# Kernel tuning notes

Hardware: AMD Instinct MI355X
Metric: run time of the kernel (lower is better)

## Reference

```python
import jax, jax.numpy as jnp
import numpy as np
import math

D_MODEL = 256
NUM_HEADS = 8
D_HEAD = 32
K_EIG = 32
NUM_BANDS = 3


def setup_inputs() -> dict:
    key = jax.random.key(0)
    ks = jax.random.split(key, 12)
    B, N = 2, 50000
    x = jax.random.normal(ks[0], (B, N, D_MODEL), dtype=jnp.float32)
    eigenvectors = jax.random.normal(ks[1], (N, K_EIG), dtype=jnp.float32) / np.sqrt(N)
    eigenvalues = jnp.sort(jax.random.uniform(ks[2], (K_EIG,), dtype=jnp.float32))
    s = 1.0 / np.sqrt(D_MODEL)
    Wq = jax.random.normal(ks[3], (NUM_HEADS * D_HEAD, D_MODEL), dtype=jnp.float32) * s
    bq = jnp.zeros((NUM_HEADS * D_HEAD,), dtype=jnp.float32)
    Wk = jax.random.normal(ks[4], (NUM_HEADS * D_HEAD, D_MODEL), dtype=jnp.float32) * s
    bk = jnp.zeros((NUM_HEADS * D_HEAD,), dtype=jnp.float32)
    Wv = jax.random.normal(ks[5], (NUM_HEADS * D_HEAD, D_MODEL), dtype=jnp.float32) * s
    bv = jnp.zeros((NUM_HEADS * D_HEAD,), dtype=jnp.float32)
    # per-head SpectralFilter params
    band_boundaries = jnp.tile(jnp.linspace(0.0, 1.0, NUM_BANDS + 1, dtype=jnp.float32)[None, :], (NUM_HEADS, 1))
    filter_weights = jnp.ones((NUM_HEADS, NUM_BANDS, K_EIG), dtype=jnp.float32) + 0.1 * jax.random.normal(ks[6], (NUM_HEADS, NUM_BANDS, K_EIG), dtype=jnp.float32)
    return {"x": x, "eigenvectors": eigenvectors, "eigenvalues": eigenvalues,
            "Wq": Wq, "bq": bq, "Wk": Wk, "bk": bk, "Wv": Wv, "bv": bv,
            "band_boundaries": band_boundaries, "filter_weights": filter_weights}


def _filter_responses(eigenvalues, band_boundaries, filter_weights):
    # eigenvalues [K]; band_boundaries [H, NB+1]; filter_weights [H, NB, K] -> [H, K]
    lam = (eigenvalues - eigenvalues.min()) / (eigenvalues.max() - eigenvalues.min() + 1e-8)  # [K]
    resp = jnp.zeros(filter_weights.shape[::2], dtype=eigenvalues.dtype)  # [H, K]
    for i in range(NUM_BANDS):  # small fixed loop; later bands overwrite (faithful to torch)
        lo = band_boundaries[:, i:i + 1]   # [H,1]
        hi = band_boundaries[:, i + 1:i + 2]
        mask = (lam[None, :] >= lo) & (lam[None, :] < hi)  # [H,K]
        resp = jnp.where(mask, filter_weights[:, i, :], resp)
    return resp


def reference(x, eigenvectors, eigenvalues, Wq, bq, Wk, bk, Wv, bv, band_boundaries, filter_weights):
    B, N, D = x.shape
    H, Dh = NUM_HEADS, D_HEAD
    Q = (x @ Wq.T + bq).reshape(B, N, H, Dh)
    K = (x @ Wk.T + bk).reshape(B, N, H, Dh)
    V = (x @ Wv.T + bv).reshape(B, N, H, Dh)
    # project to spectral domain: [B,K,H,Dh]
    Qf = jnp.einsum('nk,bnhd->bkhd', eigenvectors, Q)
    Kf = jnp.einsum('nk,bnhd->bkhd', eigenvectors, K)
    Vf = jnp.einsum('nk,bnhd->bkhd', eigenvectors, V)
    resp = _filter_responses(eigenvalues, band_boundaries, filter_weights)  # [H,K]
    g = resp.T[None, :, :, None]  # [1,K,H,1]
    Qf, Kf, Vf = Qf * g, Kf * g, Vf * g
    scores = jnp.einsum('bkhd,blhd->bkhl', Qf, Kf) / math.sqrt(Dh)  # [B,K,H,K]
    attn = jax.nn.softmax(scores, axis=-1)
    out_freq = jnp.einsum('bkhl,blhd->bkhd', attn, Vf)
    out = jnp.einsum('nk,bkhd->bnhd', eigenvectors, out_freq)
    return out.reshape(B, N, H * Dh)
```

## Files before the change

### kernel.cpp

```cpp
#include <hip/hip_runtime.h>
#include <hip/hip_bf16.h>


constexpr int D = 256;

__global__ __launch_bounds__(256) void k_colsum(const float* __restrict__ E,
                                                float* __restrict__ pS, int N) {
  int k = threadIdx.x & 31;
  int rg = threadIdx.x >> 5;
  int rs = (N + 255) >> 8;
  int n0 = blockIdx.x * rs;
  int n1 = n0 + rs; if (n1 > N) n1 = N;
  float acc = 0.f;
  for (int n = n0 + rg; n < n1; n += 8) acc += E[(size_t)n * 32 + k];
  __shared__ float red[256];
  red[threadIdx.x] = acc;
  __syncthreads();
  if (threadIdx.x < 32) {
    float t = red[threadIdx.x];
#pragma unroll
    for (int i = 1; i < 8; ++i) t += red[i * 32 + threadIdx.x];
    pS[blockIdx.x * 32 + threadIdx.x] = t;
  }
}

__global__ __launch_bounds__(256) void k_partial(const float* __restrict__ x,
                                                 const float* __restrict__ E,
                                                 float* __restrict__ pU,
                                                 int N, int nchunk, int rpc) {
  int blk = blockIdx.x;
  int dh = blk & 1;
  int bc = blk >> 1;
  int c = bc % nchunk;
  int b = bc / nchunk;
  int t = threadIdx.x;
  int ro = t >> 6;
  int lane = t & 63;
  int n0 = c * rpc;
  int n1 = n0 + rpc; if (n1 > N) n1 = N;
  int nrows = n1 - n0; if (nrows < 0) nrows = 0;

  __shared__ __align__(16) float smem[4096];

  if (nrows > 0) {
    const float4* Esrc = reinterpret_cast<const float4*>(E + (size_t)n0 * 32);
    float4* Edst = reinterpret_cast<float4*>(smem);
    int nf4 = nrows * 8;
    for (int i = t; i < nf4; i += 256) Edst[i] = Esrc[i];
  }
  __syncthreads();

  float2 a0={0,0},a1={0,0},a2={0,0},a3={0,0},a4={0,0},a5={0,0},a6={0,0},a7={0,0};
  float2 a8={0,0},a9={0,0},a10={0,0},a11={0,0},a12={0,0},a13={0,0},a14={0,0},a15={0,0};
  float2 a16={0,0},a17={0,0},a18={0,0},a19={0,0},a20={0,0},a21={0,0},a22={0,0},a23={0,0};
  float2 a24={0,0},a25={0,0},a26={0,0},a27={0,0},a28={0,0},a29={0,0},a30={0,0},a31={0,0};

  int mrows = (nrows > ro) ? ((nrows - ro + 3) >> 2) : 0;

  if (mrows > 0) {
    const float* xb = x + (size_t)b * N * D + dh * 128 + 2 * lane;
#define XLD(j) (*reinterpret_cast<const float2*>( \
    xb + (size_t)(n0 + ro + 4 * ((j) < mrows ? (j) : mrows - 1)) * D))

    float2 p0 = XLD(0), p1 = XLD(1), p2 = XLD(2), p3 = XLD(3);
    float2 p4 = XLD(4), p5 = XLD(5), p6 = XLD(6), p7 = XLD(7);

#define FMAK(e, aA, aB, aC, aD)                                   \
  aA.x = fmaf(e.x, xq.x, aA.x); aA.y = fmaf(e.x, xq.y, aA.y);     \
  aB.x = fmaf(e.y, xq.x, aB.x); aB.y = fmaf(e.y, xq.y, aB.y);     \
  aC.x = fmaf(e.z, xq.x, aC.x); aC.y = fmaf(e.z, xq.y, aC.y);     \
  aD.x = fmaf(e.w, xq.x, aD.x); aD.y = fmaf(e.w, xq.y, aD.y);

#define ROW1(j, q) {                                              \
    const float4* eb = reinterpret_cast<const float4*>(           \
        smem + (ro + 4 * (j)) * 32);                              \
    float4 e0 = eb[0], e1 = eb[1], e2 = eb[2], e3 = eb[3];        \
    float4 e4 = eb[4], e5 = eb[5], e6 = eb[6], e7 = eb[7];        \
    float2 xq = q;                                                \
    FMAK(e0, a0,  a1,  a2,  a3)  FMAK(e1, a4,  a5,  a6,  a7)      \
    FMAK(e2, a8,  a9,  a10, a11) FMAK(e3, a12, a13, a14, a15)     \
    FMAK(e4, a16, a17, a18, a19) FMAK(e5, a20, a21, a22, a23)     \
    FMAK(e6, a24, a25, a26, a27) FMAK(e7, a28, a29, a30, a31) }

    int j = 0;
#pragma unroll 1
    for (; j + 8 <= mrows; j += 8) {
      ROW1(j + 0, p0) ROW1(j + 1, p1) ROW1(j + 2, p2) ROW1(j + 3, p3)
      p0 = XLD(j + 8);  p1 = XLD(j + 9);  p2 = XLD(j + 10); p3 = XLD(j + 11);
      ROW1(j + 4, p4) ROW1(j + 5, p5) ROW1(j + 6, p6) ROW1(j + 7, p7)
      p4 = XLD(j + 12); p5 = XLD(j + 13); p6 = XLD(j + 14); p7 = XLD(j + 15);
    }
    int rem = mrows - j;
    if (rem > 0) ROW1(j + 0, p0)
    if (rem > 1) ROW1(j + 1, p1)
    if (rem > 2) ROW1(j + 2, p2)
    if (rem > 3) ROW1(j + 3, p3)
    if (rem > 4) ROW1(j + 4, p4)
    if (rem > 5) ROW1(j + 5, p5)
    if (rem > 6) ROW1(j + 6, p6)
#undef ROW1
#undef FMAK
#undef XLD
  }

  float2* rb = reinterpret_cast<float2*>(smem);
  float* o = pU + ((size_t)bc * 2 + dh) * 4096;

#define OCT(g, cA, cB, cC, cD, cE, cF, cG, cH)                    \
  __syncthreads();                                                \
  rb[(ro * 8 + 0) * 64 + lane] = cA; rb[(ro * 8 + 1) * 64 + lane] = cB; \
  rb[(ro * 8 + 2) * 64 + lane] = cC; rb[(ro * 8 + 3) * 64 + lane] = cD; \
  rb[(ro * 8 + 4) * 64 + lane] = cE; rb[(ro * 8 + 5) * 64 + lane] = cF; \
  rb[(ro * 8 + 6) * 64 + lane] = cG; rb[(ro * 8 + 7) * 64 + lane] = cH; \
  __syncthreads();                                                \
  _Pragma("unroll")                                               \
  for (int i = 0; i < 2; ++i) {                                   \
    int idx = i * 256 + t;                                        \
    int kk = idx >> 6, ll = idx & 63;                             \
    float2 s0 = rb[(0 * 8 + kk) * 64 + ll], s1 = rb[(1 * 8 + kk) * 64 + ll]; \
    float2 s2 = rb[(2 * 8 + kk) * 64 + ll], s3 = rb[(3 * 8 + kk) * 64 + ll]; \
    float2 sv;                                                    \
    sv.x = (s0.x + s1.x) + (s2.x + s3.x);                         \
    sv.y = (s0.y + s1.y) + (s2.y + s3.y);                         \
    *reinterpret_cast<float2*>(o + ((g) * 8 + kk) * 128 + 2 * ll) = sv; \
  }

  OCT(0, a0,  a1,  a2,  a3,  a4,  a5,  a6,  a7)
  OCT(1, a8,  a9,  a10, a11, a12, a13, a14, a15)
  OCT(2, a16, a17, a18, a19, a20, a21, a22, a23)
  OCT(3, a24, a25, a26, a27, a28, a29, a30, a31)
#undef OCT
}

__global__ __launch_bounds__(256) void k_reduce(const float* __restrict__ pU,
                                                float* __restrict__ U, int nchunk) {
  int e = blockIdx.x * 32 + (threadIdx.x & 31);
  int sub = threadIdx.x >> 5;
  int b = e >> 13;
  int kd = e & 8191;
  int k = kd >> 8;
  int d = kd & 255;
  int dh = d >> 7, dl = d & 127;
  const float* p = pU + (size_t)b * nchunk * 8192 + (size_t)dh * 4096 + k * 128 + dl;
  float a0 = 0.f, a1 = 0.f, a2 = 0.f, a3 = 0.f;
  float a4 = 0.f, a5 = 0.f, a6 = 0.f, a7 = 0.f;
  int c = sub;
#pragma unroll 1
  for (; c + 56 < nchunk; c += 64) {
    a0 += p[(size_t)c * 8192];
    a1 += p[(size_t)(c + 8) * 8192];
    a2 += p[(size_t)(c + 16) * 8192];
    a3 += p[(size_t)(c + 24) * 8192];
    a4 += p[(size_t)(c + 32) * 8192];
    a5 += p[(size_t)(c + 40) * 8192];
    a6 += p[(size_t)(c + 48) * 8192];
    a7 += p[(size_t)(c + 56) * 8192];
  }
  for (; c < nchunk; c += 8) a0 += p[(size_t)c * 8192];
  __shared__ float red[256];
  red[threadIdx.x] = ((a0 + a1) + (a2 + a3)) + ((a4 + a5) + (a6 + a7));
  __syncthreads();
  if (threadIdx.x < 32) {
    float s = red[threadIdx.x];
#pragma unroll
    for (int i = 1; i < 8; ++i) s += red[i * 32 + threadIdx.x];
    U[e] = s;
  }
}

__global__ __launch_bounds__(256) void k_project(
    const float* __restrict__ U, const float* __restrict__ pS,
    const float* __restrict__ Wq, const float* __restrict__ bq,
    const float* __restrict__ Wk, const float* __restrict__ bk,
    const float* __restrict__ Wv, const float* __restrict__ bv,
    const float* __restrict__ ev, const float* __restrict__ bb,
    const float* __restrict__ fw,
    float* __restrict__ Qfg, float* __restrict__ Kfg, float* __restrict__ Vfg) {
  int blk = blockIdx.x;
  int k = blk & 31;
  int t = threadIdx.x;
  __shared__ __align__(16) float u[256];
  __shared__ float red[256];
  u[t] = U[(size_t)blk * 256 + t];
  red[t] = pS[t * 32 + k];
  __syncthreads();
#pragma unroll
  for (int off = 128; off > 0; off >>= 1) {
    if (t < off) red[t] += red[t + off];
    __syncthreads();
  }
  float sk = red[0];

  float mnf = ev[0], mxf = ev[0];
#pragma unroll
  for (int i = 1; i < 32; ++i) { float v = ev[i]; mnf = fminf(mnf, v); mxf = fmaxf(mxf, v); }
  double mn = (double)mnf, mx = (double)mxf;
  double lam = ((double)ev[k] - mn) / (mx - mn + 1e-8);
  int h = t >> 5;
  float g = 0.f;
#pragma unroll
  for (int i = 0; i < 3; ++i) {
    double lo = (double)bb[h * 4 + i], hi = (double)bb[h * 4 + i + 1];
    if (lam >= lo && lam < hi) g = fw[(h * 3 + i) * 32 + k];
  }

  const float4* u4 = reinterpret_cast<const float4*>(u);
  const float4* wq4 = reinterpret_cast<const float4*>(Wq) + (size_t)t * 64;
  const float4* wk4 = reinterpret_cast<const float4*>(Wk) + (size_t)t * 64;
  const float4* wv4 = reinterpret_cast<const float4*>(Wv) + (size_t)t * 64;
  float aq = 0.f, ak = 0.f, av = 0.f;
#pragma unroll 4
  for (int j = 0; j < 64; ++j) {
    float4 uv = u4[j];
    float4 q = wq4[j], kk = wk4[j], vv = wv4[j];
    aq = fmaf(uv.x, q.x, aq);  aq = fmaf(uv.y, q.y, aq);
    aq = fmaf(uv.z, q.z, aq);  aq = fmaf(uv.w, q.w, aq);
    ak = fmaf(uv.x, kk.x, ak); ak = fmaf(uv.y, kk.y, ak);
    ak = fmaf(uv.z, kk.z, ak); ak = fmaf(uv.w, kk.w, ak);
    av = fmaf(uv.x, vv.x, av); av = fmaf(uv.y, vv.y, av);
    av = fmaf(uv.z, vv.z, av); av = fmaf(uv.w, vv.w, av);
  }
  Qfg[(size_t)blk * 256 + t] = (aq + bq[t] * sk) * g;
  Kfg[(size_t)blk * 256 + t] = (ak + bk[t] * sk) * g;
  Vfg[(size_t)blk * 256 + t] = (av + bv[t] * sk) * g;
}

__global__ __launch_bounds__(1024) void k_attn(const float* __restrict__ Qfg,
                                               const float* __restrict__ Kfg,
                                               const float* __restrict__ Vfg,
                                               float* __restrict__ of) {
  int blk = blockIdx.x;
  int b = blk >> 3, h = blk & 7;
  int tid = threadIdx.x;
  int row = tid >> 5, col = tid & 31;
  __shared__ float Q[32][33], Kt[32][33], V[32][33], A[32][33];
  size_t base = (size_t)b * 32 * 256 + h * 32;
  Q[row][col]  = Qfg[base + row * 256 + col];
  Kt[row][col] = Kfg[base + row * 256 + col];
  V[row][col]  = Vfg[base + row * 256 + col];
  __syncthreads();
  float sc = 0.f;
#pragma unroll
  for (int d0 = 0; d0 < 32; ++d0) sc = fmaf(Q[row][d0], Kt[col][d0], sc);
  sc *= 0.17677669529663687f;
  float m = sc;
#pragma unroll
  for (int o = 16; o > 0; o >>= 1) m = fmaxf(m, __shfl_xor(m, o, 32));
  float p = expf(sc - m);
  float su = p;
#pragma unroll
  for (int o = 16; o > 0; o >>= 1) su += __shfl_xor(su, o, 32);
  A[row][col] = p / su;
  __syncthreads();
  float o_ = 0.f;
#pragma unroll
  for (int l = 0; l < 32; ++l) o_ = fmaf(A[row][l], V[l][col], o_);
  of[base + row * 256 + col] = o_;
}

__global__ __launch_bounds__(256) void k_expand(const float* __restrict__ E,
                                                const float* __restrict__ of,
                                                float* __restrict__ out,
                                                int N, int rows) {
  int n0 = blockIdx.x * rows;
  int n1 = n0 + rows; if (n1 > N) n1 = N;
  int nrows = n1 - n0;
  if (nrows <= 0) return;
  int t = threadIdx.x;

  const float* ofb = of + t;
#define LDF(i) float2 f##i = make_float2(ofb[(i) * 256], ofb[8192 + (i) * 256]);
  LDF(0)  LDF(1)  LDF(2)  LDF(3)  LDF(4)  LDF(5)  LDF(6)  LDF(7)
  LDF(8)  LDF(9)  LDF(10) LDF(11) LDF(12) LDF(13) LDF(14) LDF(15)
  LDF(16) LDF(17) LDF(18) LDF(19) LDF(20) LDF(21) LDF(22) LDF(23)
  LDF(24) LDF(25) LDF(26) LDF(27) LDF(28) LDF(29) LDF(30) LDF(31)
#undef LDF

  __shared__ __align__(16) float Elds[50 * 32];
  {
    const float4* Esrc = reinterpret_cast<const float4*>(E + (size_t)n0 * 32);
    float4* Edst = reinterpret_cast<float4*>(Elds);
    int nf4 = nrows * 8;
    for (int i = t; i < nf4; i += 256) Edst[i] = Esrc[i];
  }
  __syncthreads();

  float* o0 = out + t;
  float* o1 = out + (size_t)N * D + t;

#define EXP2(s, fk) { acc0 = fmaf(s, fk.x, acc0); acc1 = fmaf(s, fk.y, acc1); }
#pragma unroll 1
  for (int i = 0; i < nrows; ++i) {
    const float4* er = reinterpret_cast<const float4*>(Elds + i * 32);
    float4 e0 = er[0], e1 = er[1], e2 = er[2], e3 = er[3];
    float4 e4 = er[4], e5 = er[5], e6 = er[6], e7 = er[7];
    float acc0 = 0.f, acc1 = 0.f;
    EXP2(e0.x, f0)  EXP2(e0.y, f1)  EXP2(e0.z, f2)  EXP2(e0.w, f3)
    EXP2(e1.x, f4)  EXP2(e1.y, f5)  EXP2(e1.z, f6)  EXP2(e1.w, f7)
    EXP2(e2.x, f8)  EXP2(e2.y, f9)  EXP2(e2.z, f10) EXP2(e2.w, f11)
    EXP2(e3.x, f12) EXP2(e3.y, f13) EXP2(e3.z, f14) EXP2(e3.w, f15)
    EXP2(e4.x, f16) EXP2(e4.y, f17) EXP2(e4.z, f18) EXP2(e4.w, f19)
    EXP2(e5.x, f20) EXP2(e5.y, f21) EXP2(e5.z, f22) EXP2(e5.w, f23)
    EXP2(e6.x, f24) EXP2(e6.y, f25) EXP2(e6.z, f26) EXP2(e6.w, f27)
    EXP2(e7.x, f28) EXP2(e7.y, f29) EXP2(e7.z, f30) EXP2(e7.w, f31)
    size_t roff = (size_t)(n0 + i) * D;
    o0[roff] = acc0;
    o1[roff] = acc1;
  }
#undef EXP2
}

extern "C" void kernel_launch(void* const* d_in, const int* in_sizes, int n_in,
                              void* d_out, int out_size, void* d_ws, size_t ws_size,
                              hipStream_t stream) {
  const float* x  = (const float*)d_in[0];
  const float* E  = (const float*)d_in[1];
  const float* ev = (const float*)d_in[2];
  const float* Wq = (const float*)d_in[3];
  const float* bq = (const float*)d_in[4];
  const float* Wk = (const float*)d_in[5];
  const float* bk = (const float*)d_in[6];
  const float* Wv = (const float*)d_in[7];
  const float* bv = (const float*)d_in[8];
  const float* bb = (const float*)d_in[9];
  const float* fw = (const float*)d_in[10];
  float* out = (float*)d_out;
  float* ws  = (float*)d_ws;

  const int N = in_sizes[1] / 32;
  const int B = in_sizes[0] / (N * 256);

  float* U   = ws;
  float* Qfg = ws + 16384;
  float* Kfg = ws + 32768;
  float* Vfg = ws + 49152;
  float* of  = ws + 65536;
  float* pS  = ws + 81920;
  float* pU  = ws + 90112;

  int nchunk = 512;
  if ((90112 + (size_t)B * nchunk * 8192) * sizeof(float) > ws_size) nchunk = 256;
  int rpc = (N + nchunk - 1) / nchunk;

  k_colsum<<<256, 256, 0, stream>>>(E, pS, N);
  k_partial<<<B * nchunk * 2, 256, 0, stream>>>(x, E, pU, N, nchunk, rpc);
  k_reduce<<<B * 8192 / 32, 256, 0, stream>>>(pU, U, nchunk);
  k_project<<<B * 32, 256, 0, stream>>>(U, pS, Wq, bq, Wk, bk, Wv, bv,
                                        ev, bb, fw, Qfg, Kfg, Vfg);
  k_attn<<<B * 8, 1024, 0, stream>>>(Qfg, Kfg, Vfg, of);
  int rows = 50;
  int nbr = (N + rows - 1) / rows;
  k_expand<<<nbr, 256, 0, stream>>>(E, of, out, N, rows);
}
```

Before: 120.4 us.

## Retile partial projection and expand kernels for float4 rows and k-split waves

The partial projection kernel now gives each block all 256 feature columns, using float4 loads of x. Its four waves are split into two k-halves times two row-parity groups, where it previously used two column halves and four row groups. This halves the block count and the number of LDS reduction rounds, and the partial buffer layout becomes contiguous so the reduce kernel indexes it directly. The expand kernel now writes float4 outputs, with waves split by batch and row parity, and rows per block go from 50 to 64. The trade-off is more accumulator registers per thread (64 floats) and fewer blocks in flight.

```diff
diff --git a/kernel.cpp b/kernel.cpp
--- a/kernel.cpp
+++ b/kernel.cpp
@@ -28,19 +28,19 @@
                                                  const float* __restrict__ E,
                                                  float* __restrict__ pU,
                                                  int N, int nchunk, int rpc) {
-  int blk = blockIdx.x;
-  int dh = blk & 1;
-  int bc = blk >> 1;
+  int bc = blockIdx.x;
   int c = bc % nchunk;
   int b = bc / nchunk;
   int t = threadIdx.x;
-  int ro = t >> 6;
+  int w = t >> 6;
+  int kh = w & 1;
+  int rp = w >> 1;
   int lane = t & 63;
   int n0 = c * rpc;
   int n1 = n0 + rpc; if (n1 > N) n1 = N;
   int nrows = n1 - n0; if (nrows < 0) nrows = 0;
 
-  __shared__ __align__(16) float smem[4096];
+  __shared__ __align__(16) float smem[8192];
 
   if (nrows > 0) {
     const float4* Esrc = reinterpret_cast<const float4*>(E + (size_t)n0 * 32);
@@ -50,86 +50,93 @@
   }
   __syncthreads();
 
-  float2 a0={0,0},a1={0,0},a2={0,0},a3={0,0},a4={0,0},a5={0,0},a6={0,0},a7={0,0};
-  float2 a8={0,0},a9={0,0},a10={0,0},a11={0,0},a12={0,0},a13={0,0},a14={0,0},a15={0,0};
-  float2 a16={0,0},a17={0,0},a18={0,0},a19={0,0},a20={0,0},a21={0,0},a22={0,0},a23={0,0};
-  float2 a24={0,0},a25={0,0},a26={0,0},a27={0,0},a28={0,0},a29={0,0},a30={0,0},a31={0,0};
-
-  int mrows = (nrows > ro) ? ((nrows - ro + 3) >> 2) : 0;
+  float4 a0={0,0,0,0},a1={0,0,0,0},a2={0,0,0,0},a3={0,0,0,0};
+  float4 a4={0,0,0,0},a5={0,0,0,0},a6={0,0,0,0},a7={0,0,0,0};
+  float4 a8={0,0,0,0},a9={0,0,0,0},a10={0,0,0,0},a11={0,0,0,0};
+  float4 a12={0,0,0,0},a13={0,0,0,0},a14={0,0,0,0},a15={0,0,0,0};
+
+  int mrows = (nrows > rp) ? ((nrows - rp + 1) >> 1) : 0;
 
   if (mrows > 0) {
-    const float* xb = x + (size_t)b * N * D + dh * 128 + 2 * lane;
-#define XLD(j) (*reinterpret_cast<const float2*>( \
-    xb + (size_t)(n0 + ro + 4 * ((j) < mrows ? (j) : mrows - 1)) * D))
-
-    float2 p0 = XLD(0), p1 = XLD(1), p2 = XLD(2), p3 = XLD(3);
-    float2 p4 = XLD(4), p5 = XLD(5), p6 = XLD(6), p7 = XLD(7);
-
-#define FMAK(e, aA, aB, aC, aD)                                   \
-  aA.x = fmaf(e.x, xq.x, aA.x); aA.y = fmaf(e.x, xq.y, aA.y);     \
-  aB.x = fmaf(e.y, xq.x, aB.x); aB.y = fmaf(e.y, xq.y, aB.y);     \
-  aC.x = fmaf(e.z, xq.x, aC.x); aC.y = fmaf(e.z, xq.y, aC.y);     \
-  aD.x = fmaf(e.w, xq.x, aD.x); aD.y = fmaf(e.w, xq.y, aD.y);
-
-#define ROW1(j, q) {                                              \
-    const float4* eb = reinterpret_cast<const float4*>(           \
-        smem + (ro + 4 * (j)) * 32);                              \
-    float4 e0 = eb[0], e1 = eb[1], e2 = eb[2], e3 = eb[3];        \
-    float4 e4 = eb[4], e5 = eb[5], e6 = eb[6], e7 = eb[7];        \
-    float2 xq = q;                                                \
-    FMAK(e0, a0,  a1,  a2,  a3)  FMAK(e1, a4,  a5,  a6,  a7)      \
-    FMAK(e2, a8,  a9,  a10, a11) FMAK(e3, a12, a13, a14, a15)     \
-    FMAK(e4, a16, a17, a18, a19) FMAK(e5, a20, a21, a22, a23)     \
-    FMAK(e6, a24, a25, a26, a27) FMAK(e7, a28, a29, a30, a31) }
+    const float* xb = x + (size_t)b * N * D + 4 * lane;
+#define XLD(j) (*reinterpret_cast<const float4*>( \
+    xb + (size_t)(n0 + rp + 2 * ((j) < mrows ? (j) : mrows - 1)) * D))
+
+    float4 p0 = XLD(0), p1 = XLD(1), p2 = XLD(2), p3 = XLD(3);
+    float4 p4 = XLD(4), p5 = XLD(5), p6 = XLD(6), p7 = XLD(7);
+
+#define FK(s, A) { A.x = fmaf(s, xq.x, A.x); A.y = fmaf(s, xq.y, A.y); \
+                   A.z = fmaf(s, xq.z, A.z); A.w = fmaf(s, xq.w, A.w); }
+#define ROWP(j, q) {                                               \
+    const float4* eb = reinterpret_cast<const float4*>(            \
+        smem + (rp + 2 * (j)) * 32 + kh * 16);                     \
+    float4 e0 = eb[0], e1 = eb[1], e2 = eb[2], e3 = eb[3];         \
+    float4 xq = q;                                                 \
+    FK(e0.x, a0)  FK(e0.y, a1)  FK(e0.z, a2)  FK(e0.w, a3)         \
+    FK(e1.x, a4)  FK(e1.y, a5)  FK(e1.z, a6)  FK(e1.w, a7)         \
+    FK(e2.x, a8)  FK(e2.y, a9)  FK(e2.z, a10) FK(e2.w, a11)        \
+    FK(e3.x, a12) FK(e3.y, a13) FK(e3.z, a14) FK(e3.w, a15) }
 
     int j = 0;
 #pragma unroll 1
     for (; j + 8 <= mrows; j += 8) {
-      ROW1(j + 0, p0) ROW1(j + 1, p1) ROW1(j + 2, p2) ROW1(j + 3, p3)
+      ROWP(j + 0, p0) ROWP(j + 1, p1) ROWP(j + 2, p2) ROWP(j + 3, p3)
       p0 = XLD(j + 8);  p1 = XLD(j + 9);  p2 = XLD(j + 10); p3 = XLD(j + 11);
-      ROW1(j + 4, p4) ROW1(j + 5, p5) ROW1(j + 6, p6) ROW1(j + 7, p7)
+      ROWP(j + 4, p4) ROWP(j + 5, p5) ROWP(j + 6, p6) ROWP(j + 7, p7)
       p4 = XLD(j + 12); p5 = XLD(j + 13); p6 = XLD(j + 14); p7 = XLD(j + 15);
     }
     int rem = mrows - j;
-    if (rem > 0) ROW1(j + 0, p0)
-    if (rem > 1) ROW1(j + 1, p1)
-    if (rem > 2) ROW1(j + 2, p2)
-    if (rem > 3) ROW1(j + 3, p3)
-    if (rem > 4) ROW1(j + 4, p4)
-    if (rem > 5) ROW1(j + 5, p5)
-    if (rem > 6) ROW1(j + 6, p6)
-#undef ROW1
-#undef FMAK
+    if (rem > 0) ROWP(j + 0, p0)
+    if (rem > 1) ROWP(j + 1, p1)
+    if (rem > 2) ROWP(j + 2, p2)
+    if (rem > 3) ROWP(j + 3, p3)
+    if (rem > 4) ROWP(j + 4, p4)
+    if (rem > 5) ROWP(j + 5, p5)
+    if (rem > 6) ROWP(j + 6, p6)
+#undef ROWP
+#undef FK
 #undef XLD
   }
 
-  float2* rb = reinterpret_cast<float2*>(smem);
-  float* o = pU + ((size_t)bc * 2 + dh) * 4096;
-
-#define OCT(g, cA, cB, cC, cD, cE, cF, cG, cH)                    \
-  __syncthreads();                                                \
-  rb[(ro * 8 + 0) * 64 + lane] = cA; rb[(ro * 8 + 1) * 64 + lane] = cB; \
-  rb[(ro * 8 + 2) * 64 + lane] = cC; rb[(ro * 8 + 3) * 64 + lane] = cD; \
-  rb[(ro * 8 + 4) * 64 + lane] = cE; rb[(ro * 8 + 5) * 64 + lane] = cF; \
-  rb[(ro * 8 + 6) * 64 + lane] = cG; rb[(ro * 8 + 7) * 64 + lane] = cH; \
-  __syncthreads();                                                \
-  _Pragma("unroll")                                               \
-  for (int i = 0; i < 2; ++i) {                                   \
-    int idx = i * 256 + t;                                        \
-    int kk = idx >> 6, ll = idx & 63;                             \
-    float2 s0 = rb[(0 * 8 + kk) * 64 + ll], s1 = rb[(1 * 8 + kk) * 64 + ll]; \
-    float2 s2 = rb[(2 * 8 + kk) * 64 + ll], s3 = rb[(3 * 8 + kk) * 64 + ll]; \
-    float2 sv;                                                    \
-    sv.x = (s0.x + s1.x) + (s2.x + s3.x);                         \
-    sv.y = (s0.y + s1.y) + (s2.y + s3.y);                         \
-    *reinterpret_cast<float2*>(o + ((g) * 8 + kk) * 128 + 2 * ll) = sv; \
-  }
-
-  OCT(0, a0,  a1,  a2,  a3,  a4,  a5,  a6,  a7)
-  OCT(1, a8,  a9,  a10, a11, a12, a13, a14, a15)
-  OCT(2, a16, a17, a18, a19, a20, a21, a22, a23)
-  OCT(3, a24, a25, a26, a27, a28, a29, a30, a31)
-#undef OCT
+  float4* buf = reinterpret_cast<float4*>(smem);
+  float* ob = pU + (size_t)bc * 8192 + (size_t)(kh * 16) * 256 + 4 * lane;
+
+#define REDP(koff, A0, A1, A2, A3, A4, A5, A6, A7)                 \
+  __syncthreads();                                                 \
+  if (rp == 1) {                                                   \
+    buf[(kh * 8 + 0) * 64 + lane] = A0;                            \
+    buf[(kh * 8 + 1) * 64 + lane] = A1;                            \
+    buf[(kh * 8 + 2) * 64 + lane] = A2;                            \
+    buf[(kh * 8 + 3) * 64 + lane] = A3;                            \
+    buf[(kh * 8 + 4) * 64 + lane] = A4;                            \
+    buf[(kh * 8 + 5) * 64 + lane] = A5;                            \
+    buf[(kh * 8 + 6) * 64 + lane] = A6;                            \
+    buf[(kh * 8 + 7) * 64 + lane] = A7;                            \
+  }                                                                \
+  __syncthreads();                                                 \
+  if (rp == 0) {                                                   \
+    float4 s;                                                      \
+    s = buf[(kh*8+0)*64+lane]; A0.x+=s.x; A0.y+=s.y; A0.z+=s.z; A0.w+=s.w; \
+    *reinterpret_cast<float4*>(ob + ((koff)+0)*256) = A0;          \
+    s = buf[(kh*8+1)*64+lane]; A1.x+=s.x; A1.y+=s.y; A1.z+=s.z; A1.w+=s.w; \
+    *reinterpret_cast<float4*>(ob + ((koff)+1)*256) = A1;          \
+    s = buf[(kh*8+2)*64+lane]; A2.x+=s.x; A2.y+=s.y; A2.z+=s.z; A2.w+=s.w; \
+    *reinterpret_cast<float4*>(ob + ((koff)+2)*256) = A2;          \
+    s = buf[(kh*8+3)*64+lane]; A3.x+=s.x; A3.y+=s.y; A3.z+=s.z; A3.w+=s.w; \
+    *reinterpret_cast<float4*>(ob + ((koff)+3)*256) = A3;          \
+    s = buf[(kh*8+4)*64+lane]; A4.x+=s.x; A4.y+=s.y; A4.z+=s.z; A4.w+=s.w; \
+    *reinterpret_cast<float4*>(ob + ((koff)+4)*256) = A4;          \
+    s = buf[(kh*8+5)*64+lane]; A5.x+=s.x; A5.y+=s.y; A5.z+=s.z; A5.w+=s.w; \
+    *reinterpret_cast<float4*>(ob + ((koff)+5)*256) = A5;          \
+    s = buf[(kh*8+6)*64+lane]; A6.x+=s.x; A6.y+=s.y; A6.z+=s.z; A6.w+=s.w; \
+    *reinterpret_cast<float4*>(ob + ((koff)+6)*256) = A6;          \
+    s = buf[(kh*8+7)*64+lane]; A7.x+=s.x; A7.y+=s.y; A7.z+=s.z; A7.w+=s.w; \
+    *reinterpret_cast<float4*>(ob + ((koff)+7)*256) = A7;          \
+  }
+
+  REDP(0, a0, a1, a2, a3, a4, a5, a6, a7)
+  REDP(8, a8, a9, a10, a11, a12, a13, a14, a15)
+#undef REDP
 }
 
 __global__ __launch_bounds__(256) void k_reduce(const float* __restrict__ pU,
@@ -138,10 +145,7 @@
   int sub = threadIdx.x >> 5;
   int b = e >> 13;
   int kd = e & 8191;
-  int k = kd >> 8;
-  int d = kd & 255;
-  int dh = d >> 7, dl = d & 127;
-  const float* p = pU + (size_t)b * nchunk * 8192 + (size_t)dh * 4096 + k * 128 + dl;
+  const float* p = pU + (size_t)b * nchunk * 8192 + kd;
   float a0 = 0.f, a1 = 0.f, a2 = 0.f, a3 = 0.f;
   float a4 = 0.f, a5 = 0.f, a6 = 0.f, a7 = 0.f;
   int c = sub;
@@ -267,16 +271,20 @@
   int nrows = n1 - n0;
   if (nrows <= 0) return;
   int t = threadIdx.x;
-
-  const float* ofb = of + t;
-#define LDF(i) float2 f##i = make_float2(ofb[(i) * 256], ofb[8192 + (i) * 256]);
+  int w = t >> 6;
+  int bb = w & 1;
+  int rp = w >> 1;
+  int lane = t & 63;
+
+  const float* ofb = of + (size_t)bb * 8192 + 4 * lane;
+#define LDF(i) float4 f##i = *reinterpret_cast<const float4*>(ofb + (i) * 256);
   LDF(0)  LDF(1)  LDF(2)  LDF(3)  LDF(4)  LDF(5)  LDF(6)  LDF(7)
   LDF(8)  LDF(9)  LDF(10) LDF(11) LDF(12) LDF(13) LDF(14) LDF(15)
   LDF(16) LDF(17) LDF(18) LDF(19) LDF(20) LDF(21) LDF(22) LDF(23)
   LDF(24) LDF(25) LDF(26) LDF(27) LDF(28) LDF(29) LDF(30) LDF(31)
 #undef LDF
 
-  __shared__ __align__(16) float Elds[50 * 32];
+  __shared__ __align__(16) float Elds[64 * 32];
   {
     const float4* Esrc = reinterpret_cast<const float4*>(E + (size_t)n0 * 32);
     float4* Edst = reinterpret_cast<float4*>(Elds);
@@ -285,29 +293,30 @@
   }
   __syncthreads();
 
-  float* o0 = out + t;
-  float* o1 = out + (size_t)N * D + t;
-
-#define EXP2(s, fk) { acc0 = fmaf(s, fk.x, acc0); acc1 = fmaf(s, fk.y, acc1); }
+  float* ob = out + (size_t)bb * N * D + 4 * lane;
+
+#define EX(s, fk, A) { A.x = fmaf(s, fk.x, A.x); A.y = fmaf(s, fk.y, A.y); \
+                       A.z = fmaf(s, fk.z, A.z); A.w = fmaf(s, fk.w, A.w); }
 #pragma unroll 1
-  for (int i = 0; i < nrows; ++i) {
+  for (int i = rp; i < nrows; i += 2) {
     const float4* er = reinterpret_cast<const float4*>(Elds + i * 32);
     float4 e0 = er[0], e1 = er[1], e2 = er[2], e3 = er[3];
     float4 e4 = er[4], e5 = er[5], e6 = er[6], e7 = er[7];
-    float acc0 = 0.f, acc1 = 0.f;
-    EXP2(e0.x, f0)  EXP2(e0.y, f1)  EXP2(e0.z, f2)  EXP2(e0.w, f3)
-    EXP2(e1.x, f4)  EXP2(e1.y, f5)  EXP2(e1.z, f6)  EXP2(e1.w, f7)
-    EXP2(e2.x, f8)  EXP2(e2.y, f9)  EXP2(e2.z, f10) EXP2(e2.w, f11)
-    EXP2(e3.x, f12) EXP2(e3.y, f13) EXP2(e3.z, f14) EXP2(e3.w, f15)
-    EXP2(e4.x, f16) EXP2(e4.y, f17) EXP2(e4.z, f18) EXP2(e4.w, f19)
-    EXP2(e5.x, f20) EXP2(e5.y, f21) EXP2(e5.z, f22) EXP2(e5.w, f23)
-    EXP2(e6.x, f24) EXP2(e6.y, f25) EXP2(e6.z, f26) EXP2(e6.w, f27)
-    EXP2(e7.x, f28) EXP2(e7.y, f29) EXP2(e7.z, f30) EXP2(e7.w, f31)
-    size_t roff = (size_t)(n0 + i) * D;
-    o0[roff] = acc0;
-    o1[roff] = acc1;
-  }
-#undef EXP2
+    float4 oA = {0.f, 0.f, 0.f, 0.f}, oB = {0.f, 0.f, 0.f, 0.f};
+    EX(e0.x, f0,  oA) EX(e0.y, f1,  oB) EX(e0.z, f2,  oA) EX(e0.w, f3,  oB)
+    EX(e1.x, f4,  oA) EX(e1.y, f5,  oB) EX(e1.z, f6,  oA) EX(e1.w, f7,  oB)
+    EX(e2.x, f8,  oA) EX(e2.y, f9,  oB) EX(e2.z, f10, oA) EX(e2.w, f11, oB)
+    EX(e3.x, f12, oA) EX(e3.y, f13, oB) EX(e3.z, f14, oA) EX(e3.w, f15, oB)
+    EX(e4.x, f16, oA) EX(e4.y, f17, oB) EX(e4.z, f18, oA) EX(e4.w, f19, oB)
+    EX(e5.x, f20, oA) EX(e5.y, f21, oB) EX(e5.z, f22, oA) EX(e5.w, f23, oB)
+    EX(e6.x, f24, oA) EX(e6.y, f25, oB) EX(e6.z, f26, oA) EX(e6.w, f27, oB)
+    EX(e7.x, f28, oA) EX(e7.y, f29, oB) EX(e7.z, f30, oA) EX(e7.w, f31, oB)
+    float4 o4;
+    o4.x = oA.x + oB.x; o4.y = oA.y + oB.y;
+    o4.z = oA.z + oB.z; o4.w = oA.w + oB.w;
+    *reinterpret_cast<float4*>(ob + (size_t)(n0 + i) * D) = o4;
+  }
+#undef EX
 }
 
 extern "C" void kernel_launch(void* const* d_in, const int* in_sizes, int n_in,
@@ -343,12 +352,12 @@
   int rpc = (N + nchunk - 1) / nchunk;
 
   k_colsum<<<256, 256, 0, stream>>>(E, pS, N);
-  k_partial<<<B * nchunk * 2, 256, 0, stream>>>(x, E, pU, N, nchunk, rpc);
+  k_partial<<<B * nchunk, 256, 0, stream>>>(x, E, pU, N, nchunk, rpc);
   k_reduce<<<B * 8192 / 32, 256, 0, stream>>>(pU, U, nchunk);
   k_project<<<B * 32, 256, 0, stream>>>(U, pS, Wq, bq, Wk, bk, Wv, bv,
                                         ev, bb, fw, Qfg, Kfg, Vfg);
   k_attn<<<B * 8, 1024, 0, stream>>>(Qfg, Kfg, Vfg, of);
-  int rows = 50;
+  int rows = 64;
   int nbr = (N + rows - 1) / rows;
   k_expand<<<nbr, 256, 0, stream>>>(E, of, out, N, rows);
 }
```

New measurement: 162.3 us. 1.35x slower.
